# Optimization experiments

Hardware: AMD Instinct MI355X
Metric: run time of the kernel (lower is better)

The kernel has to match this reference:

```python
import jax, jax.numpy as jnp
import numpy as np

N = 50000      # nodes
E = 800000     # edges (avg degree 16)
DIN = 256
DOUT = 256
EA = 16        # edge_attr_dim
EH = 32        # edge_mlp_hidden
Z = 0.8        # z_ratio
EPS = 1e-5


def _lin_init(k, fin, fout):
    k1, k2 = jax.random.split(k)
    s = 1.0 / np.sqrt(fin)
    W = jax.random.uniform(k1, (fin, fout), jnp.float32, -s, s)
    b = jax.random.uniform(k2, (fout,), jnp.float32, -s, s)
    return W, b


def setup_inputs() -> dict:
    key = jax.random.key(0)
    ks = jax.random.split(key, 12)
    x = jax.random.normal(ks[0], (N, DIN), dtype=jnp.float32)
    edge_index = jax.random.randint(ks[1], (2, E), 0, N, dtype=jnp.int64)
    edge_weight = jax.random.uniform(ks[2], (E,), dtype=jnp.float32)
    mask = jax.random.bernoulli(ks[3], 0.5, (N, 1))
    edge_attr = jax.random.normal(ks[4], (E, EA), dtype=jnp.float32)
    Wt0, bt0 = _lin_init(ks[5], DIN, DOUT)
    Wt1, bt1 = _lin_init(ks[6], DIN, DOUT)
    Wc0, bc0 = _lin_init(ks[7], DIN + DOUT, DOUT)
    Wc1, bc1 = _lin_init(ks[8], DIN + DOUT, DOUT)
    gn_w = jnp.ones((DOUT,), jnp.float32)
    gn_b = jnp.zeros((DOUT,), jnp.float32)
    gn_alpha = jnp.ones((DOUT,), jnp.float32)  # GraphNorm mean_scale
    Wm1, bm1 = _lin_init(ks[9], EA, EH)
    Wm2, bm2 = _lin_init(ks[10], EH, 1)
    return {
        'x': x, 'edge_index': edge_index, 'edge_weight': edge_weight,
        'mask': mask, 'edge_attr': edge_attr,
        'Wt0': Wt0, 'bt0': bt0, 'Wt1': Wt1, 'bt1': bt1,
        'Wc0': Wc0, 'bc0': bc0, 'Wc1': Wc1, 'bc1': bc1,
        'gn_w': gn_w, 'gn_b': gn_b, 'gn_alpha': gn_alpha,
        'Wm1': Wm1, 'bm1': bm1, 'Wm2': Wm2, 'bm2': bm2,
    }


def _mix(m, a1, a0):
    # torch.where(mask, z*x1 + (1-z)*x0, z*x0 + (1-z)*x1)
    return jnp.where(m, Z * a1 + (1.0 - Z) * a0, Z * a0 + (1.0 - Z) * a1)


def reference(x, edge_index, edge_weight, mask, edge_attr,
              Wt0, bt0, Wt1, bt1, Wc0, bc0, Wc1, bc1,
              gn_w, gn_b, gn_alpha, Wm1, bm1, Wm2, bm2):
    n_node = x.shape[0]
    row, col = edge_index[0], edge_index[1]

    # edge MLP (scalar mode): edge_weight <- softplus(MLP(edge_attr))
    h = jax.nn.relu(edge_attr @ Wm1 + bm1)
    ew = jax.nn.softplus((h @ Wm2 + bm2))[:, 0]  # [E]

    # buildAdj with aggr='mean': row-normalized weights
    deg = jax.ops.segment_sum(ew, row, num_segments=n_node)
    deg = jnp.where(deg < 0.5, deg + 1.0, deg)
    w = ew / deg[row]  # [E]

    # dual-branch transform + masked mix
    x1 = jax.nn.relu(x @ Wt1 + bt1)
    x0 = jax.nn.relu(x @ Wt0 + bt0)
    xm = _mix(mask, x1, x0)  # [N, DOUT]

    # sparse adj @ x : gather at col, scatter-add at row
    agg = jax.ops.segment_sum(w[:, None] * xm[col], row, num_segments=n_node)

    # GraphNorm (single graph): x - alpha*mean, normalize by std
    mean = jnp.mean(agg, axis=0)
    out = agg - gn_alpha * mean
    var = jnp.mean(out * out, axis=0)
    out = gn_w * out * jax.lax.rsqrt(var + EPS) + gn_b

    # dropout inactive in eval mode
    xc = jnp.concatenate([out, x], axis=-1)  # [N, DOUT+DIN]
    c1 = xc @ Wc1 + bc1
    c0 = xc @ Wc0 + bc0
    return _mix(mask, c1, c0)
```

## Files before the change

kernel.cpp:

```cpp
#include <hip/hip_runtime.h>

#define NN 50000
#define NE 800000
#define NNP 50176

#define OFF_START 200704
#define OFF_BSUM  401408
#define OFF_S1    402432
#define OFF_S2    403456
#define OFF_WTT1  404480
#define OFF_WTT0  535552
#define OFF_WTC1  666624
#define OFF_WTC0  928768
#define OFF_RANK  1190912
#define OFF_COLW  4390912
#define OFF_XMB   10790912
#define OFF_AGG   36481024
#define OFF_XBF   62171136
#define OFF_B1F   10790912
#define OFF_B0F   10791936

typedef __attribute__((ext_vector_type(4))) float f32x4;
typedef __bf16 bf16x8 __attribute__((ext_vector_type(8)));

__device__ __forceinline__ float bfu2f(unsigned short u) {
  return __uint_as_float(((unsigned)u) << 16);
}
__device__ __forceinline__ unsigned short f2bf(float f) {
  unsigned u = __float_as_uint(f);
  u += 0x7fffu + ((u >> 16) & 1u);
  return (unsigned short)(u >> 16);
}

__device__ __forceinline__ void gload16(const void* g, void* l) {
  __builtin_amdgcn_global_load_lds(
      (const __attribute__((address_space(1))) unsigned int*)g,
      (__attribute__((address_space(3))) unsigned int*)l, 16, 0, 0);
}

__global__ __launch_bounds__(256) void prep_kernel(
    const float* __restrict__ X, unsigned short* __restrict__ xbf,
    const int* __restrict__ ei, int* __restrict__ cnt, int* __restrict__ rank,
    const float* __restrict__ Wt1, const float* __restrict__ Wt0,
    const float* __restrict__ Wc1, const float* __restrict__ Wc0,
    unsigned short* __restrict__ WTt1, unsigned short* __restrict__ WTt0,
    unsigned short* __restrict__ WTc1, unsigned short* __restrict__ WTc0,
    unsigned short* __restrict__ aggb) {
  __shared__ unsigned short T[32 * 40];
  const int bid = blockIdx.x;
  const int t = threadIdx.x;
  if (bid < 3125) {
    const int e = bid * 256 + t;
    if (e < NE) rank[e] = atomicAdd(&cnt[ei[e]], 1);
    return;
  }
  if (bid < 3125 + 6272) {
    const int gid = (bid - 3125) * 256 + t;
    const long base = (long)gid * 8;
    const int row = (int)(base >> 8);
    unsigned short o[8];
    if (row < NN) {
      f32x4 a = *(const f32x4*)(X + base);
      f32x4 b = *(const f32x4*)(X + base + 4);
#pragma unroll
      for (int i = 0; i < 4; i++) { o[i] = f2bf(a[i]); o[4 + i] = f2bf(b[i]); }
    } else {
#pragma unroll
      for (int i = 0; i < 8; i++) o[i] = 0;
    }
    *(uint4*)(xbf + base) = *(const uint4*)o;
    return;
  }
  if (bid < 3125 + 6272 + 384) {
    int tb = bid - (3125 + 6272);
    const float* W;
    unsigned short* WT;
    int K, kx, ny;
    if (tb < 64) { W = Wt1; WT = WTt1; K = 256; kx = tb & 7; ny = tb >> 3; }
    else if (tb < 128) { tb -= 64; W = Wt0; WT = WTt0; K = 256; kx = tb & 7; ny = tb >> 3; }
    else if (tb < 256) { tb -= 128; W = Wc1; WT = WTc1; K = 512; kx = tb & 15; ny = tb >> 4; }
    else { tb -= 256; W = Wc0; WT = WTc0; K = 512; kx = tb & 15; ny = tb >> 4; }
    const int k0 = kx * 32, n0 = ny * 32;
    const int kk = t >> 3, nn = (t & 7) * 4;
    f32x4 v = *(const f32x4*)(W + (k0 + kk) * 256 + n0 + nn);
#pragma unroll
    for (int i = 0; i < 4; i++) T[(nn + i) * 40 + kk] = f2bf(v[i]);
    __syncthreads();
    const int nn2 = t >> 3, kk2 = (t & 7) * 4;
    unsigned short o[4];
#pragma unroll
    for (int i = 0; i < 4; i++) o[i] = T[nn2 * 40 + kk2 + i];
    *(uint2*)(WT + (n0 + nn2) * K + k0 + kk2) = *(const uint2*)o;
    return;
  }
  const int idx = (bid - (3125 + 6272 + 384)) * 256 + t;
  if (idx < 5632) ((uint4*)(aggb + (size_t)NN * 256))[idx] = make_uint4(0, 0, 0, 0);
}

__global__ __launch_bounds__(256) void scan1_kernel(const int* __restrict__ cnt,
                                                    int* __restrict__ blockSum) {
  __shared__ int sd[256];
  const int t = threadIdx.x;
  sd[t] = cnt[blockIdx.x * 256 + t];
  __syncthreads();
  for (int off = 128; off > 0; off >>= 1) {
    if (t < off) sd[t] += sd[t + off];
    __syncthreads();
  }
  if (t == 0) blockSum[blockIdx.x] = sd[0];
}

__global__ __launch_bounds__(256) void scan23_kernel(
    const int* __restrict__ cnt, const int* __restrict__ blockSum,
    int* __restrict__ start) {
  __shared__ int sd[256];
  __shared__ int pfx;
  const int t = threadIdx.x;
  const int bid = blockIdx.x;
  int v = (t < 196) ? blockSum[t] : 0;
  sd[t] = v;
  __syncthreads();
  for (int off = 1; off < 256; off <<= 1) {
    int y = (t >= off) ? sd[t - off] : 0;
    __syncthreads();
    sd[t] += y;
    __syncthreads();
  }
  if (t == 0) pfx = (bid == 0) ? 0 : sd[bid - 1];
  __syncthreads();
  const int row = bid * 256 + t;
  const int c = cnt[row];
  sd[t] = c;
  __syncthreads();
  for (int off = 1; off < 256; off <<= 1) {
    int y = (t >= off) ? sd[t - off] : 0;
    __syncthreads();
    sd[t] += y;
    __syncthreads();
  }
  start[row] = pfx + sd[t] - c;
}

__device__ __forceinline__ void mlp4(float a0, float a1, float a2, float a3,
                                     const f32x4* __restrict__ w,
                                     f32x4& h0, f32x4& h1, f32x4& h2, f32x4& h3,
                                     f32x4& h4, f32x4& h5, f32x4& h6, f32x4& h7) {
  h0 += w[0] * a0;  h1 += w[1] * a0;  h2 += w[2] * a0;  h3 += w[3] * a0;
  h4 += w[4] * a0;  h5 += w[5] * a0;  h6 += w[6] * a0;  h7 += w[7] * a0;
  h0 += w[8] * a1;  h1 += w[9] * a1;  h2 += w[10] * a1; h3 += w[11] * a1;
  h4 += w[12] * a1; h5 += w[13] * a1; h6 += w[14] * a1; h7 += w[15] * a1;
  h0 += w[16] * a2; h1 += w[17] * a2; h2 += w[18] * a2; h3 += w[19] * a2;
  h4 += w[20] * a2; h5 += w[21] * a2; h6 += w[22] * a2; h7 += w[23] * a2;
  h0 += w[24] * a3; h1 += w[25] * a3; h2 += w[26] * a3; h3 += w[27] * a3;
  h4 += w[28] * a3; h5 += w[29] * a3; h6 += w[30] * a3; h7 += w[31] * a3;
}

__device__ __forceinline__ float rdot(f32x4 h, f32x4 w) {
  float s = fmaxf(h[0], 0.0f) * w[0];
  s = fmaf(fmaxf(h[1], 0.0f), w[1], s);
  s = fmaf(fmaxf(h[2], 0.0f), w[2], s);
  s = fmaf(fmaxf(h[3], 0.0f), w[3], s);
  return s;
}

template <int KTOT, bool SPLIT, bool OUT_BF16>
__device__ __forceinline__ void gemm_tile(unsigned short* SH, int task,
    const unsigned short* __restrict__ A0, const unsigned short* __restrict__ A1,
    const unsigned short* __restrict__ WT1, const unsigned short* __restrict__ WT0,
    const float* __restrict__ bias1, const float* __restrict__ bias0,
    const int* __restrict__ mask, void* __restrict__ outp) {
  unsigned short* Al  = SH;
  unsigned short* B1l = SH + 8192;
  unsigned short* B0l = SH + 12288;
  const int t = threadIdx.x;
  const int swz = (task & 7) * 196 + (task >> 3);
  const int bx = swz & 3, by = swz >> 2;
  const int row0 = by * 128, col0 = bx * 64;
  const int wv = t >> 6, lane = t & 63, m = lane & 15, q = lane >> 4;
  const int wr = wv >> 1, wc = wv & 1;
  const int arow = t >> 3, ach = t & 7;
  f32x4 acc1[4][2], acc0[4][2];
#pragma unroll
  for (int rf = 0; rf < 4; rf++)
#pragma unroll
    for (int nt = 0; nt < 2; nt++) { acc1[rf][nt] = (f32x4)(0.0f); acc0[rf][nt] = (f32x4)(0.0f); }

  for (int k0 = 0; k0 < KTOT; k0 += 64) {
    const unsigned short* Ab;
    int kr;
    if constexpr (SPLIT) {
      if (k0 < 256) { Ab = A0; kr = k0; } else { Ab = A1; kr = k0 - 256; }
    } else { Ab = A0; kr = k0; }
#pragma unroll
    for (int i = 0; i < 4; i++) {
      const int r = arow + i * 32;
      gload16(Ab + (size_t)(row0 + r) * 256 + kr + ((ach ^ (r & 7)) << 3),
              &Al[(i * 256 + t) * 8]);
    }
#pragma unroll
    for (int i = 0; i < 2; i++) {
      const int r = arow + i * 32;
      const int sc = (ach ^ (r & 7)) << 3;
      gload16(WT1 + (size_t)(col0 + r) * KTOT + k0 + sc, &B1l[(i * 256 + t) * 8]);
      gload16(WT0 + (size_t)(col0 + r) * KTOT + k0 + sc, &B0l[(i * 256 + t) * 8]);
    }
    __syncthreads();
#pragma unroll
    for (int kk = 0; kk < 2; kk++) {
      bf16x8 af[4];
#pragma unroll
      for (int rf = 0; rf < 4; rf++) {
        const int r = wr * 64 + rf * 16 + m;
        af[rf] = *(const bf16x8*)&Al[r * 64 + (((kk * 4 + q) ^ (r & 7)) << 3)];
      }
#pragma unroll
      for (int nt = 0; nt < 2; nt++) {
        const int n = wc * 32 + nt * 16 + m;
        const int off = n * 64 + (((kk * 4 + q) ^ (n & 7)) << 3);
        bf16x8 f1 = *(const bf16x8*)&B1l[off];
        bf16x8 f0 = *(const bf16x8*)&B0l[off];
#pragma unroll
        for (int rf = 0; rf < 4; rf++) {
          acc1[rf][nt] = __builtin_amdgcn_mfma_f32_16x16x32_bf16(af[rf], f1, acc1[rf][nt], 0, 0, 0);
          acc0[rf][nt] = __builtin_amdgcn_mfma_f32_16x16x32_bf16(af[rf], f0, acc0[rf][nt], 0, 0, 0);
        }
      }
    }
    __syncthreads();
  }

#pragma unroll
  for (int rf = 0; rf < 4; rf++) {
    const int rbase = row0 + wr * 64 + rf * 16 + q * 4;
    int mk[4];
#pragma unroll
    for (int r = 0; r < 4; r++) mk[r] = (rbase + r < NN) ? mask[rbase + r] : 0;
#pragma unroll
    for (int nt = 0; nt < 2; nt++) {
      const int gc = col0 + wc * 32 + nt * 16 + m;
      const float bb1 = bias1[gc];
      const float bb0 = bias0[gc];
#pragma unroll
      for (int r = 0; r < 4; r++) {
        const int grr = rbase + r;
        if (grr < NN) {
          float v1 = acc1[rf][nt][r] + bb1;
          float v0 = acc0[rf][nt][r] + bb0;
          if constexpr (OUT_BF16) {
            v1 = fmaxf(v1, 0.0f);
            v0 = fmaxf(v0, 0.0f);
            float o = mk[r] ? (0.8f * v1 + 0.2f * v0) : (0.8f * v0 + 0.2f * v1);
            ((unsigned short*)outp)[(size_t)grr * 256 + gc] = f2bf(o);
          } else {
            float o = mk[r] ? (0.8f * v1 + 0.2f * v0) : (0.8f * v0 + 0.2f * v1);
            ((float*)outp)[(size_t)grr * 256 + gc] = o;
          }
        }
      }
    }
  }
}

__global__ __launch_bounds__(256, 3) void midk(
    const unsigned short* __restrict__ xbf,
    const unsigned short* __restrict__ WTt1, const unsigned short* __restrict__ WTt0,
    const float* __restrict__ bt1, const float* __restrict__ bt0,
    const int* __restrict__ msk, unsigned short* __restrict__ xmb,
    const float* __restrict__ ea,
    const float* __restrict__ Wm1, const float* __restrict__ bm1,
    const float* __restrict__ Wm2, const float* __restrict__ bm2,
    const int* __restrict__ ei, const int* __restrict__ start,
    const int* __restrict__ rank, uint2* __restrict__ colw) {
  __shared__ __align__(16) unsigned short SH[128 * 64 + 64 * 64 + 64 * 64];
  const int bid = blockIdx.x;
  const int t = threadIdx.x;
  if (bid < 1568) {
    gemm_tile<256, false, true>(SH, bid, xbf, (const unsigned short*)nullptr,
                                WTt1, WTt0, bt1, bt0, msk, xmb);
    return;
  }
  float* w1 = (float*)SH;
  float* b1 = w1 + 512;
  float* w2 = b1 + 32;
  float* b2s = w2 + 32;
  w1[t] = Wm1[t];
  w1[t + 256] = Wm1[t + 256];
  if (t < 32) { b1[t] = bm1[t]; w2[t] = Wm2[t]; }
  if (t == 0) b2s[0] = bm2[0];
  __syncthreads();
  const int e = (bid - 1568) * 256 + t;
  if (e >= NE) return;
  f32x4 r0 = *(const f32x4*)(ea + e * 16);
  f32x4 r1 = *(const f32x4*)(ea + e * 16 + 4);
  f32x4 r2 = *(const f32x4*)(ea + e * 16 + 8);
  f32x4 r3 = *(const f32x4*)(ea + e * 16 + 12);
  const f32x4* bv = (const f32x4*)b1;
  f32x4 h0 = bv[0], h1 = bv[1], h2 = bv[2], h3 = bv[3];
  f32x4 h4 = bv[4], h5 = bv[5], h6 = bv[6], h7 = bv[7];
  const f32x4* wv = (const f32x4*)w1;
  mlp4(r0[0], r0[1], r0[2], r0[3], wv, h0, h1, h2, h3, h4, h5, h6, h7);
  mlp4(r1[0], r1[1], r1[2], r1[3], wv + 32, h0, h1, h2, h3, h4, h5, h6, h7);
  mlp4(r2[0], r2[1], r2[2], r2[3], wv + 64, h0, h1, h2, h3, h4, h5, h6, h7);
  mlp4(r3[0], r3[1], r3[2], r3[3], wv + 96, h0, h1, h2, h3, h4, h5, h6, h7);
  const f32x4* w2v = (const f32x4*)w2;
  float s = b2s[0];
  s += rdot(h0, w2v[0]) + rdot(h1, w2v[1]) + rdot(h2, w2v[2]) + rdot(h3, w2v[3]);
  s += rdot(h4, w2v[4]) + rdot(h5, w2v[5]) + rdot(h6, w2v[6]) + rdot(h7, w2v[7]);
  const float sp = (s > 0.0f) ? (s + log1pf(expf(-s))) : log1pf(expf(s));
  uint2 p;
  p.x = (unsigned)ei[NE + e];
  p.y = __float_as_uint(sp);
  colw[start[ei[e]] + rank[e]] = p;
}

__global__ __launch_bounds__(256, 3) void gemm_combine(
    const unsigned short* __restrict__ aggb, const unsigned short* __restrict__ xbf,
    const unsigned short* __restrict__ WT1, const unsigned short* __restrict__ WT0,
    const float* __restrict__ bias1, const float* __restrict__ bias0,
    const int* __restrict__ mask, float* __restrict__ out) {
  __shared__ __align__(16) unsigned short SH[128 * 64 + 64 * 64 + 64 * 64];
  const int task = blockIdx.y * gridDim.x + blockIdx.x;
  gemm_tile<512, true, false>(SH, task, aggb, xbf, WT1, WT0, bias1, bias0, mask, out);
}

#define EDGE(u, wgt) do { \
  dsum += wgt; \
  acc[0] = fmaf(wgt, __uint_as_float(u.x << 16), acc[0]); \
  acc[1] = fmaf(wgt, __uint_as_float(u.x & 0xffff0000u), acc[1]); \
  acc[2] = fmaf(wgt, __uint_as_float(u.y << 16), acc[2]); \
  acc[3] = fmaf(wgt, __uint_as_float(u.y & 0xffff0000u), acc[3]); \
} while (0)

__global__ __launch_bounds__(256) void aggregate_kernel(
    const int* __restrict__ start, const int* __restrict__ cnt,
    const uint2* __restrict__ colw,
    const unsigned short* __restrict__ xmb, unsigned short* __restrict__ aggb) {
  const int wave = threadIdx.x >> 6, lane = threadIdx.x & 63;
  const int row = blockIdx.x * 4 + wave;
  const int s = start[row];
  const int c = cnt[row];
  const int choff = lane * 4;
  f32x4 acc = (f32x4)(0.0f);
  float dsum = 0.0f;
  int i = 0;
  for (; i + 8 <= c; i += 8) {
    uint2 cw0 = colw[s + i],     cw1 = colw[s + i + 1];
    uint2 cw2 = colw[s + i + 2], cw3 = colw[s + i + 3];
    uint2 cw4 = colw[s + i + 4], cw5 = colw[s + i + 5];
    uint2 cw6 = colw[s + i + 6], cw7 = colw[s + i + 7];
    uint2 u0 = *(const uint2*)(xmb + (size_t)cw0.x * 256 + choff);
    uint2 u1 = *(const uint2*)(xmb + (size_t)cw1.x * 256 + choff);
    uint2 u2 = *(const uint2*)(xmb + (size_t)cw2.x * 256 + choff);
    uint2 u3 = *(const uint2*)(xmb + (size_t)cw3.x * 256 + choff);
    uint2 u4 = *(const uint2*)(xmb + (size_t)cw4.x * 256 + choff);
    uint2 u5 = *(const uint2*)(xmb + (size_t)cw5.x * 256 + choff);
    uint2 u6 = *(const uint2*)(xmb + (size_t)cw6.x * 256 + choff);
    uint2 u7 = *(const uint2*)(xmb + (size_t)cw7.x * 256 + choff);
    EDGE(u0, __uint_as_float(cw0.y));
    EDGE(u1, __uint_as_float(cw1.y));
    EDGE(u2, __uint_as_float(cw2.y));
    EDGE(u3, __uint_as_float(cw3.y));
    EDGE(u4, __uint_as_float(cw4.y));
    EDGE(u5, __uint_as_float(cw5.y));
    EDGE(u6, __uint_as_float(cw6.y));
    EDGE(u7, __uint_as_float(cw7.y));
  }
  for (; i + 4 <= c; i += 4) {
    uint2 cw0 = colw[s + i],     cw1 = colw[s + i + 1];
    uint2 cw2 = colw[s + i + 2], cw3 = colw[s + i + 3];
    uint2 u0 = *(const uint2*)(xmb + (size_t)cw0.x * 256 + choff);
    uint2 u1 = *(const uint2*)(xmb + (size_t)cw1.x * 256 + choff);
    uint2 u2 = *(const uint2*)(xmb + (size_t)cw2.x * 256 + choff);
    uint2 u3 = *(const uint2*)(xmb + (size_t)cw3.x * 256 + choff);
    EDGE(u0, __uint_as_float(cw0.y));
    EDGE(u1, __uint_as_float(cw1.y));
    EDGE(u2, __uint_as_float(cw2.y));
    EDGE(u3, __uint_as_float(cw3.y));
  }
  for (; i < c; i++) {
    uint2 cw0 = colw[s + i];
    uint2 u0 = *(const uint2*)(xmb + (size_t)cw0.x * 256 + choff);
    EDGE(u0, __uint_as_float(cw0.y));
  }
  float d = (dsum < 0.5f) ? dsum + 1.0f : dsum;
  const float inv = 1.0f / d;
  unsigned short o[4];
#pragma unroll
  for (int j = 0; j < 4; j++) o[j] = f2bf(acc[j] * inv);
  *(uint2*)(aggb + (size_t)row * 256 + choff) = *(const uint2*)o;
}

__global__ __launch_bounds__(256) void stats_kernel(
    const unsigned short* __restrict__ aggb, float* __restrict__ S1, float* __restrict__ S2) {
  const int c = threadIdx.x;
  const int r0 = blockIdx.x * 200;
  float s1 = 0.0f, s2 = 0.0f;
  for (int r = 0; r < 200; r++) {
    float v = bfu2f(aggb[(size_t)(r0 + r) * 256 + c]);
    s1 += v;
    s2 = fmaf(v, v, s2);
  }
  unsafeAtomicAdd(&S1[c], s1);
  unsafeAtomicAdd(&S2[c], s2);
}

__global__ __launch_bounds__(256) void fold_kernel(
    const float* __restrict__ S1, const float* __restrict__ S2,
    const float* __restrict__ gnw, const float* __restrict__ gnb,
    const float* __restrict__ gna,
    const float* __restrict__ Wc1, const float* __restrict__ Wc0,
    const float* __restrict__ bc1, const float* __restrict__ bc0,
    unsigned short* __restrict__ WTc1, unsigned short* __restrict__ WTc0,
    float* __restrict__ b1f, float* __restrict__ b0f) {
  __shared__ float r1[256];
  __shared__ float r0[256];
  const int n = blockIdx.x, t = threadIdx.x;
  const float inv_n = 1.0f / (float)NN;
  const float mean = S1[t] * inv_n;
  const float ex2 = S2[t] * inv_n;
  const float am = gna[t] * mean;
  const float var = ex2 - 2.0f * am * mean + am * am;
  const float sc = gnw[t] * rsqrtf(var + 1e-5f);
  const float sh = gnb[t] - sc * am;
  const float w1 = bfu2f(WTc1[n * 512 + t]);
  WTc1[n * 512 + t] = f2bf(w1 * sc);
  const float w0 = bfu2f(WTc0[n * 512 + t]);
  WTc0[n * 512 + t] = f2bf(w0 * sc);
  r1[t] = sh * Wc1[t * 256 + n];
  r0[t] = sh * Wc0[t * 256 + n];
  __syncthreads();
  for (int off = 128; off > 0; off >>= 1) {
    if (t < off) { r1[t] += r1[t + off]; r0[t] += r0[t + off]; }
    __syncthreads();
  }
  if (t == 0) {
    b1f[n] = bc1[n] + r1[0];
    b0f[n] = bc0[n] + r0[0];
  }
}

extern "C" void kernel_launch(void* const* d_in, const int* in_sizes, int n_in,
                              void* d_out, int out_size, void* d_ws, size_t ws_size,
                              hipStream_t stream) {
  (void)in_sizes; (void)n_in; (void)out_size; (void)ws_size;
  const float* x   = (const float*)d_in[0];
  const int*   ei  = (const int*)d_in[1];
  const int*   msk = (const int*)d_in[3];
  const float* ea  = (const float*)d_in[4];
  const float* Wt0 = (const float*)d_in[5];
  const float* bt0 = (const float*)d_in[6];
  const float* Wt1 = (const float*)d_in[7];
  const float* bt1 = (const float*)d_in[8];
  const float* Wc0 = (const float*)d_in[9];
  const float* bc0 = (const float*)d_in[10];
  const float* Wc1 = (const float*)d_in[11];
  const float* bc1 = (const float*)d_in[12];
  const float* gnw = (const float*)d_in[13];
  const float* gnb = (const float*)d_in[14];
  const float* gna = (const float*)d_in[15];
  const float* Wm1 = (const float*)d_in[16];
  const float* bm1 = (const float*)d_in[17];
  const float* Wm2 = (const float*)d_in[18];
  const float* bm2 = (const float*)d_in[19];

  char* ws = (char*)d_ws;
  int* cnt      = (int*)ws;
  int* startA   = (int*)(ws + OFF_START);
  int* blockSum = (int*)(ws + OFF_BSUM);
  float* S1     = (float*)(ws + OFF_S1);
  float* S2     = (float*)(ws + OFF_S2);
  unsigned short* WTt1 = (unsigned short*)(ws + OFF_WTT1);
  unsigned short* WTt0 = (unsigned short*)(ws + OFF_WTT0);
  unsigned short* WTc1 = (unsigned short*)(ws + OFF_WTC1);
  unsigned short* WTc0 = (unsigned short*)(ws + OFF_WTC0);
  int* rankA    = (int*)(ws + OFF_RANK);
  uint2* colw   = (uint2*)(ws + OFF_COLW);
  unsigned short* xmb  = (unsigned short*)(ws + OFF_XMB);
  unsigned short* aggb = (unsigned short*)(ws + OFF_AGG);
  unsigned short* xbf  = (unsigned short*)(ws + OFF_XBF);
  float* b1f = (float*)(ws + OFF_B1F);
  float* b0f = (float*)(ws + OFF_B0F);

  hipMemsetAsync(ws, 0, 404480, stream);

  prep_kernel<<<9803, 256, 0, stream>>>(x, xbf, ei, cnt, rankA,
                                        Wt1, Wt0, Wc1, Wc0,
                                        WTt1, WTt0, WTc1, WTc0, aggb);
  scan1_kernel<<<196, 256, 0, stream>>>(cnt, blockSum);
  scan23_kernel<<<196, 256, 0, stream>>>(cnt, blockSum, startA);
  midk<<<4693, 256, 0, stream>>>(xbf, WTt1, WTt0, bt1, bt0, msk, xmb,
                                 ea, Wm1, bm1, Wm2, bm2, ei, startA, rankA, colw);
  aggregate_kernel<<<12500, 256, 0, stream>>>(startA, cnt, colw, xmb, aggb);
  stats_kernel<<<250, 256, 0, stream>>>(aggb, S1, S2);
  fold_kernel<<<256, 256, 0, stream>>>(S1, S2, gnw, gnb, gna, Wc1, Wc0, bc1, bc0,
                                       WTc1, WTc0, b1f, b0f);
  gemm_combine<<<dim3(4, 392), 256, 0, stream>>>(aggb, xbf, WTc1, WTc0, b1f, b0f,
                                                 msk, (float*)d_out);
}
```

Measured before the change: 376.7 us.

## Widen GEMM tiles to 128x128 and merge the two-pass scan into one kernel

Each GEMM block now computes a 128x128 output tile for both branches, with 4x4 MFMA fragments per wave, instead of 128x64. This halves the number of times the A operand is reloaded per output, at the cost of more registers and LDS (occupancy bound lowered to 2). The block-sum scan pass is folded into the prefix kernel: every block recomputes all block sums directly from cnt, which removes one launch but duplicates a small amount of reads.

New measurement: 384.3 us. +2.0%, slower.

```diff
diff --git a/kernel.cpp b/kernel.cpp
--- a/kernel.cpp
+++ b/kernel.cpp
@@ -97,28 +97,21 @@
   if (idx < 5632) ((uint4*)(aggb + (size_t)NN * 256))[idx] = make_uint4(0, 0, 0, 0);
 }
 
-__global__ __launch_bounds__(256) void scan1_kernel(const int* __restrict__ cnt,
-                                                    int* __restrict__ blockSum) {
-  __shared__ int sd[256];
-  const int t = threadIdx.x;
-  sd[t] = cnt[blockIdx.x * 256 + t];
-  __syncthreads();
-  for (int off = 128; off > 0; off >>= 1) {
-    if (t < off) sd[t] += sd[t + off];
-    __syncthreads();
-  }
-  if (t == 0) blockSum[blockIdx.x] = sd[0];
-}
-
-__global__ __launch_bounds__(256) void scan23_kernel(
-    const int* __restrict__ cnt, const int* __restrict__ blockSum,
-    int* __restrict__ start) {
+__global__ __launch_bounds__(256) void scan_all(
+    const int* __restrict__ cnt, int* __restrict__ start) {
   __shared__ int sd[256];
   __shared__ int pfx;
   const int t = threadIdx.x;
   const int bid = blockIdx.x;
-  int v = (t < 196) ? blockSum[t] : 0;
-  sd[t] = v;
+  int s = 0;
+  if (t < 196) {
+    const int* p = cnt + t * 256;
+    for (int j = 0; j < 256; j += 4) {
+      int4 v = *(const int4*)(p + j);
+      s += v.x + v.y + v.z + v.w;
+    }
+  }
+  sd[t] = s;
   __syncthreads();
   for (int off = 1; off < 256; off <<= 1) {
     int y = (t >= off) ? sd[t - off] : 0;
@@ -171,19 +164,19 @@
     const int* __restrict__ mask, void* __restrict__ outp) {
   unsigned short* Al  = SH;
   unsigned short* B1l = SH + 8192;
-  unsigned short* B0l = SH + 12288;
+  unsigned short* B0l = SH + 16384;
   const int t = threadIdx.x;
-  const int swz = (task & 7) * 196 + (task >> 3);
-  const int bx = swz & 3, by = swz >> 2;
-  const int row0 = by * 128, col0 = bx * 64;
+  const int swz = (task & 7) * 98 + (task >> 3);
+  const int bx = swz & 1, by = swz >> 1;
+  const int row0 = by * 128, col0 = bx * 128;
   const int wv = t >> 6, lane = t & 63, m = lane & 15, q = lane >> 4;
   const int wr = wv >> 1, wc = wv & 1;
   const int arow = t >> 3, ach = t & 7;
-  f32x4 acc1[4][2], acc0[4][2];
+  f32x4 acc1[4][4], acc0[4][4];
 #pragma unroll
   for (int rf = 0; rf < 4; rf++)
 #pragma unroll
-    for (int nt = 0; nt < 2; nt++) { acc1[rf][nt] = (f32x4)(0.0f); acc0[rf][nt] = (f32x4)(0.0f); }
+    for (int nt = 0; nt < 4; nt++) { acc1[rf][nt] = (f32x4)(0.0f); acc0[rf][nt] = (f32x4)(0.0f); }
 
   for (int k0 = 0; k0 < KTOT; k0 += 64) {
     const unsigned short* Ab;
@@ -198,7 +191,7 @@
               &Al[(i * 256 + t) * 8]);
     }
 #pragma unroll
-    for (int i = 0; i < 2; i++) {
+    for (int i = 0; i < 4; i++) {
       const int r = arow + i * 32;
       const int sc = (ach ^ (r & 7)) << 3;
       gload16(WT1 + (size_t)(col0 + r) * KTOT + k0 + sc, &B1l[(i * 256 + t) * 8]);
@@ -214,8 +207,8 @@
         af[rf] = *(const bf16x8*)&Al[r * 64 + (((kk * 4 + q) ^ (r & 7)) << 3)];
       }
 #pragma unroll
-      for (int nt = 0; nt < 2; nt++) {
-        const int n = wc * 32 + nt * 16 + m;
+      for (int nt = 0; nt < 4; nt++) {
+        const int n = wc * 64 + nt * 16 + m;
         const int off = n * 64 + (((kk * 4 + q) ^ (n & 7)) << 3);
         bf16x8 f1 = *(const bf16x8*)&B1l[off];
         bf16x8 f0 = *(const bf16x8*)&B0l[off];
@@ -236,8 +229,8 @@
 #pragma unroll
     for (int r = 0; r < 4; r++) mk[r] = (rbase + r < NN) ? mask[rbase + r] : 0;
 #pragma unroll
-    for (int nt = 0; nt < 2; nt++) {
-      const int gc = col0 + wc * 32 + nt * 16 + m;
+    for (int nt = 0; nt < 4; nt++) {
+      const int gc = col0 + wc * 64 + nt * 16 + m;
       const float bb1 = bias1[gc];
       const float bb0 = bias0[gc];
 #pragma unroll
@@ -261,7 +254,7 @@
   }
 }
 
-__global__ __launch_bounds__(256, 3) void midk(
+__global__ __launch_bounds__(256, 2) void midk(
     const unsigned short* __restrict__ xbf,
     const unsigned short* __restrict__ WTt1, const unsigned short* __restrict__ WTt0,
     const float* __restrict__ bt1, const float* __restrict__ bt0,
@@ -271,10 +264,10 @@
     const float* __restrict__ Wm2, const float* __restrict__ bm2,
     const int* __restrict__ ei, const int* __restrict__ start,
     const int* __restrict__ rank, uint2* __restrict__ colw) {
-  __shared__ __align__(16) unsigned short SH[128 * 64 + 64 * 64 + 64 * 64];
+  __shared__ __align__(16) unsigned short SH[3 * 128 * 64];
   const int bid = blockIdx.x;
   const int t = threadIdx.x;
-  if (bid < 1568) {
+  if (bid < 784) {
     gemm_tile<256, false, true>(SH, bid, xbf, (const unsigned short*)nullptr,
                                 WTt1, WTt0, bt1, bt0, msk, xmb);
     return;
@@ -288,7 +281,7 @@
   if (t < 32) { b1[t] = bm1[t]; w2[t] = Wm2[t]; }
   if (t == 0) b2s[0] = bm2[0];
   __syncthreads();
-  const int e = (bid - 1568) * 256 + t;
+  const int e = (bid - 784) * 256 + t;
   if (e >= NE) return;
   f32x4 r0 = *(const f32x4*)(ea + e * 16);
   f32x4 r1 = *(const f32x4*)(ea + e * 16 + 4);
@@ -313,14 +306,13 @@
   colw[start[ei[e]] + rank[e]] = p;
 }
 
-__global__ __launch_bounds__(256, 3) void gemm_combine(
+__global__ __launch_bounds__(256, 2) void gemm_combine(
     const unsigned short* __restrict__ aggb, const unsigned short* __restrict__ xbf,
     const unsigned short* __restrict__ WT1, const unsigned short* __restrict__ WT0,
     const float* __restrict__ bias1, const float* __restrict__ bias0,
     const int* __restrict__ mask, float* __restrict__ out) {
-  __shared__ __align__(16) unsigned short SH[128 * 64 + 64 * 64 + 64 * 64];
-  const int task = blockIdx.y * gridDim.x + blockIdx.x;
-  gemm_tile<512, true, false>(SH, task, aggb, xbf, WT1, WT0, bias1, bias0, mask, out);
+  __shared__ __align__(16) unsigned short SH[3 * 128 * 64];
+  gemm_tile<512, true, false>(SH, blockIdx.x, aggb, xbf, WT1, WT0, bias1, bias0, mask, out);
 }
 
 #define EDGE(u, wgt) do { \
@@ -466,7 +458,6 @@
   char* ws = (char*)d_ws;
   int* cnt      = (int*)ws;
   int* startA   = (int*)(ws + OFF_START);
-  int* blockSum = (int*)(ws + OFF_BSUM);
   float* S1     = (float*)(ws + OFF_S1);
   float* S2     = (float*)(ws + OFF_S2);
   unsigned short* WTt1 = (unsigned short*)(ws + OFF_WTT1);
@@ -486,14 +477,13 @@
   prep_kernel<<<9803, 256, 0, stream>>>(x, xbf, ei, cnt, rankA,
                                         Wt1, Wt0, Wc1, Wc0,
                                         WTt1, WTt0, WTc1, WTc0, aggb);
-  scan1_kernel<<<196, 256, 0, stream>>>(cnt, blockSum);
-  scan23_kernel<<<196, 256, 0, stream>>>(cnt, blockSum, startA);
-  midk<<<4693, 256, 0, stream>>>(xbf, WTt1, WTt0, bt1, bt0, msk, xmb,
+  scan_all<<<196, 256, 0, stream>>>(cnt, startA);
+  midk<<<3909, 256, 0, stream>>>(xbf, WTt1, WTt0, bt1, bt0, msk, xmb,
                                  ea, Wm1, bm1, Wm2, bm2, ei, startA, rankA, colw);
   aggregate_kernel<<<12500, 256, 0, stream>>>(startA, cnt, colw, xmb, aggb);
   stats_kernel<<<250, 256, 0, stream>>>(aggb, S1, S2);
   fold_kernel<<<256, 256, 0, stream>>>(S1, S2, gnw, gnb, gna, Wc1, Wc0, bc1, bc0,
                                        WTc1, WTc0, b1f, b0f);
-  gemm_combine<<<dim3(4, 392), 256, 0, stream>>>(aggb, xbf, WTc1, WTc0, b1f, b0f,
-                                                 msk, (float*)d_out);
-}
+  gemm_combine<<<784, 256, 0, stream>>>(aggb, xbf, WTc1, WTc0, b1f, b0f,
+                                        msk, (float*)d_out);
+}
```
